# Optimization experiments

Hardware: AMD Instinct MI355X
Metric: run time of the kernel (lower is better)

The kernel has to match this reference:

```python
import jax, jax.numpy as jnp
import numpy as np

S = 2048      # sequence length
D = 2048      # d_model
H = 16        # n_heads
E = 128       # d_head


def setup_inputs() -> dict:
    key = jax.random.key(0)
    kx, kw = jax.random.split(key)
    x = jax.random.normal(kx, (S, D), dtype=jnp.float32)
    # xavier_normal for fan_in=D, fan_out=3*E per head
    std = float(np.sqrt(2.0 / (D + 3 * E)))
    w_qkv = jax.random.normal(kw, (H, D, 3 * E), dtype=jnp.float32) * std
    return {"x": x, "w_qkv": w_qkv}


def reference(x, w_qkv):
    # qkv: [h, s, 3e]
    qkv = jnp.einsum('sd,hde->hse', x, w_qkv)
    q, k, v = jnp.split(qkv, 3, axis=-1)            # each [h, s, e]
    scores = jnp.einsum('hse,hte->hst', q, k) / jnp.sqrt(jnp.asarray(E, x.dtype))
    attn = jax.nn.softmax(scores, axis=-1)          # [h, s, t]
    out = jnp.einsum('hst,hte->hse', attn, v)       # [h, s, e]
    # concat heads: [s, h*e]
    return out.transpose(1, 0, 2).reshape(x.shape[0], -1)
```

## Files before the change

### kernel.cpp

```cpp
#include <hip/hip_runtime.h>

#define SEQ 2048
#define DMODEL 2048
#define NHEAD 16
#define EHEAD 128
#define NE3 384

using short8 = __attribute__((ext_vector_type(8))) short;
using f32x4  = __attribute__((ext_vector_type(4))) float;
using f32x16 = __attribute__((ext_vector_type(16))) float;
using uint4v = __attribute__((ext_vector_type(4))) unsigned int;
using uint2v = __attribute__((ext_vector_type(2))) unsigned int;

__device__ __forceinline__ unsigned short f32_to_bf16(float f) {
    unsigned int u = __float_as_uint(f);
    unsigned int rounding = 0x7fffu + ((u >> 16) & 1u);
    u += rounding;
    return (unsigned short)(u >> 16);
}

__device__ __forceinline__ void async_load16(const void* g, void* l) {
    __builtin_amdgcn_global_load_lds(
        (const __attribute__((address_space(1))) unsigned int*)g,
        (__attribute__((address_space(3))) unsigned int*)l, 16, 0, 0);
}

__global__ void prep_kernel(const float* __restrict__ x, unsigned short* __restrict__ xb,
                            const float* __restrict__ w, unsigned short* __restrict__ wT) {
    __shared__ float tile[64][65];
    const int bid = blockIdx.x;
    if (bid < 4096) {
        int i = (bid * blockDim.x + threadIdx.x) * 4;
        float4 v = *(const float4*)(x + i);
        ushort4 o = make_ushort4(f32_to_bf16(v.x), f32_to_bf16(v.y), f32_to_bf16(v.z), f32_to_bf16(v.w));
        *(ushort4*)(xb + i) = o;
        return;
    }
    const int b = bid - 4096;
    const int h  = b / 192;
    const int r6 = b % 192;
    const int n0 = (r6 / 32) * 64;
    const int d0 = (r6 % 32) * 64;
    int t = threadIdx.x;
    int rr = t >> 4;
    int cc = (t & 15) * 4;
#pragma unroll
    for (int i = 0; i < 4; i++) {
        float4 v = *(const float4*)&w[(size_t)(h * DMODEL + d0 + rr + i * 16) * NE3 + n0 + cc];
        tile[rr + i * 16][cc + 0] = v.x;
        tile[rr + i * 16][cc + 1] = v.y;
        tile[rr + i * 16][cc + 2] = v.z;
        tile[rr + i * 16][cc + 3] = v.w;
    }
    __syncthreads();
#pragma unroll
    for (int i = 0; i < 4; i++) {
        int n = rr + i * 16;
        ushort4 o;
        o.x = f32_to_bf16(tile[cc + 0][n]);
        o.y = f32_to_bf16(tile[cc + 1][n]);
        o.z = f32_to_bf16(tile[cc + 2][n]);
        o.w = f32_to_bf16(tile[cc + 3][n]);
        *(ushort4*)&wT[(size_t)(h * NE3 + n0 + n) * DMODEL + d0 + cc] = o;
    }
}

template <int B, bool STAGE, int VM, bool RDNEXT>
__device__ __forceinline__ void qkv_kstep(
        unsigned short* lds, f32x4 (&acc)[4][6],
        short8 (&aC)[4], short8 (&bC)[3],
        short8 (&aN)[4], short8 (&bN)[3],
        const unsigned short*& p0, const unsigned short*& p1,
        const unsigned short*& p2, const unsigned short*& p3,
        const int d0, const int d1, const int d2, const int d3,
        const int aoff, const int boff) {
    constexpr int CUR = B * 16384;
    constexpr int NXT = ((B + 1) & 3) * 16384;
    constexpr int DST = ((B + 3) & 3) * 16384;

    short8 b1[3];
#pragma unroll
    for (int nf = 0; nf < 3; ++nf) b1[nf] = *(const short8*)(lds + CUR + boff + (3 + nf) * 512);
    if constexpr (STAGE) {
        async_load16(p0, lds + DST + d0);
        async_load16(p1, lds + DST + d1);
    }
    p0 += 32; p1 += 32;
    if constexpr (VM == 6)      asm volatile("s_waitcnt vmcnt(6)");
    else if constexpr (VM == 4) asm volatile("s_waitcnt vmcnt(4)");
    else if constexpr (VM == 0) asm volatile("s_waitcnt vmcnt(0)");
    __builtin_amdgcn_s_barrier();
    __builtin_amdgcn_s_setprio(1);
#pragma unroll
    for (int mf = 0; mf < 4; ++mf)
#pragma unroll
        for (int nf = 0; nf < 3; ++nf)
            acc[mf][nf] = __builtin_amdgcn_mfma_f32_16x16x32_bf16(aC[mf], bC[nf], acc[mf][nf], 0, 0, 0);
    __builtin_amdgcn_s_setprio(0);
    __builtin_amdgcn_s_barrier();

    if constexpr (RDNEXT) {
#pragma unroll
        for (int mf = 0; mf < 4; ++mf) aN[mf] = *(const short8*)(lds + NXT + aoff + mf * 512);
#pragma unroll
        for (int nf = 0; nf < 3; ++nf) bN[nf] = *(const short8*)(lds + NXT + boff + nf * 512);
    }
    if constexpr (STAGE) {
        async_load16(p2, lds + DST + d2);
        async_load16(p3, lds + DST + d3);
    }
    p2 += 32; p3 += 32;
    __builtin_amdgcn_s_barrier();
    __builtin_amdgcn_s_setprio(1);
#pragma unroll
    for (int mf = 0; mf < 4; ++mf)
#pragma unroll
        for (int nf = 0; nf < 3; ++nf)
            acc[mf][3 + nf] = __builtin_amdgcn_mfma_f32_16x16x32_bf16(aC[mf], b1[nf], acc[mf][3 + nf], 0, 0, 0);
    __builtin_amdgcn_s_setprio(0);
    __builtin_amdgcn_s_barrier();
}

__global__ __launch_bounds__(512, 2) void qkv_gemm384(
        const unsigned short* __restrict__ A,
        const unsigned short* __restrict__ Bm,
        unsigned short* __restrict__ Q,
        unsigned short* __restrict__ Kb,
        unsigned short* __restrict__ Vt) {
    extern __shared__ __attribute__((aligned(16))) unsigned short lds[];
    const int mb = blockIdx.x, nb = blockIdx.y;
    const int tid = threadIdx.x;
    const int wave = tid >> 6, lane = tid & 63;
    const int r = lane & 15, q = lane >> 4;
    const int wm = wave >> 2, wn = wave & 3;

    const int rrm  = (tid >> 2) & 15;
    const int kg   = ((tid & 3) ^ ((rrm >> 1) & 3)) * 8;
    const int rowA = ((tid >> 6) << 4) + rrm;
    const unsigned short* p0 = A  + (size_t)(mb * 128 + rowA) * DMODEL + kg;
    const unsigned short* p1 = Bm + (size_t)(nb * 384 + rowA) * DMODEL + kg;
    const unsigned short* p2 = p1 + (size_t)128 * DMODEL;
    const unsigned short* p3 = p1 + (size_t)256 * DMODEL;
    const int d0 = wave * 512;
    const int d1 = 4096 + wave * 512;
    const int d2 = 8192 + wave * 512;
    const int d3 = 12288 + wave * 512;

#pragma unroll
    for (int t = 0; t < 3; ++t) {
        async_load16(p0 + t * 32, lds + t * 16384 + d0);
        async_load16(p1 + t * 32, lds + t * 16384 + d1);
        async_load16(p2 + t * 32, lds + t * 16384 + d2);
        async_load16(p3 + t * 32, lds + t * 16384 + d3);
    }
    p0 += 96; p1 += 96; p2 += 96; p3 += 96;

    const int qs = q ^ ((r >> 1) & 3);
    const int aoff = wm * 2048 + r * 32 + qs * 8;
    const int boff = 4096 + wn * 3072 + r * 32 + qs * 8;

    f32x4 acc[4][6] = {};
    asm volatile("s_waitcnt vmcnt(8)");
    __builtin_amdgcn_s_barrier();

    short8 aA[4], bA[3], aB[4], bB[3];
#pragma unroll
    for (int mf = 0; mf < 4; ++mf) aA[mf] = *(const short8*)(lds + aoff + mf * 512);
#pragma unroll
    for (int nf = 0; nf < 3; ++nf) bA[nf] = *(const short8*)(lds + boff + nf * 512);

    for (int i = 0; i < 15; ++i) {
        qkv_kstep<0, true, 6, true>(lds, acc, aA, bA, aB, bB, p0, p1, p2, p3, d0, d1, d2, d3, aoff, boff);
        qkv_kstep<1, true, 6, true>(lds, acc, aB, bB, aA, bA, p0, p1, p2, p3, d0, d1, d2, d3, aoff, boff);
        qkv_kstep<2, true, 6, true>(lds, acc, aA, bA, aB, bB, p0, p1, p2, p3, d0, d1, d2, d3, aoff, boff);
        qkv_kstep<3, true, 6, true>(lds, acc, aB, bB, aA, bA, p0, p1, p2, p3, d0, d1, d2, d3, aoff, boff);
    }
    qkv_kstep<0, true,  6, true >(lds, acc, aA, bA, aB, bB, p0, p1, p2, p3, d0, d1, d2, d3, aoff, boff);
    qkv_kstep<1, false, 4, true >(lds, acc, aB, bB, aA, bA, p0, p1, p2, p3, d0, d1, d2, d3, aoff, boff);
    qkv_kstep<2, false, 0, true >(lds, acc, aA, bA, aB, bB, p0, p1, p2, p3, d0, d1, d2, d3, aoff, boff);
    qkv_kstep<3, false, -1, false>(lds, acc, aB, bB, aA, bA, p0, p1, p2, p3, d0, d1, d2, d3, aoff, boff);

    const int head = nb;
    const int mbase = mb * 128 + wm * 64;
#pragma unroll
    for (int nf = 0; nf < 6; ++nf) {
        const int cb = wn * 96 + nf * 16;
        const int sel = cb >> 7;
        const int e = (cb & 127) + r;
#pragma unroll
        for (int mf = 0; mf < 4; ++mf) {
            const int row0 = mbase + mf * 16 + q * 4;
            const f32x4 v = acc[mf][nf];
            if (sel == 2) {
                ushort4 o;
                o.x = f32_to_bf16(v[0]);
                o.y = f32_to_bf16(v[1]);
                o.z = f32_to_bf16(v[2]);
                o.w = f32_to_bf16(v[3]);
                *(ushort4*)&Vt[((size_t)head * EHEAD + e) * SEQ + row0] = o;
            } else {
                unsigned short* dst = sel ? Kb : Q;
#pragma unroll
                for (int reg = 0; reg < 4; ++reg)
                    dst[((size_t)head * SEQ + row0 + reg) * EHEAD + e] = f32_to_bf16(v[reg]);
            }
        }
    }
}

__global__ __launch_bounds__(512, 2) void flash_attn(
        const unsigned short* __restrict__ Qg,
        const unsigned short* __restrict__ Kg,
        const unsigned short* __restrict__ Vtg,
        float* __restrict__ out) {
    extern __shared__ __attribute__((aligned(16))) unsigned short lds[];
    unsigned short* sK0 = lds;
    unsigned short* sV0 = lds + 16384;

    const int tid = threadIdx.x;
    const int wave = tid >> 6, lane = tid & 63;
    const int l31 = lane & 31, q2 = lane >> 5;
    const int wm = wave >> 1, wn = wave & 1;
    const int b = blockIdx.x;
    const int h  = (b & 7) + ((b >> 7) << 3);
    const int m0 = ((b >> 3) & 15) * 128;

    const unsigned short* Qh  = Qg  + ((size_t)h * SEQ + m0) * EHEAD;
    const unsigned short* Kh0 = Kg  + (size_t)h * SEQ * EHEAD;
    const unsigned short* Vh  = Vtg + (size_t)h * EHEAD * SEQ;

    const int qkRow = lane >> 4;
    const int qkPos = lane & 15;
    const int vRow  = lane >> 3;
    const int vPos  = lane & 7;

    const unsigned short* gK[2];
    const unsigned short* gV[2];
#pragma unroll
    for (int c = 0; c < 2; c++) {
        int u = wave * 2 + c;
        int row = u * 4 + qkRow;
        int ch = qkPos ^ (row & 7);
        gK[c] = Kh0 + (size_t)row * EHEAD + ch * 8;
        int rv = u * 8 + vRow;
        int cv = vPos ^ (rv & 7);
        gV[c] = Vh + (size_t)rv * SEQ + cv * 8;
        async_load16(gK[c], sK0 + u * 512);
        async_load16(gV[c], sV0 + u * 512);
        gK[c] += 64 * EHEAD;
        gV[c] += 64;
    }

    short8 bq[8];
    {
        const unsigned short* qrow = Qh + (size_t)(wm * 32 + l31) * EHEAD;
#pragma unroll
        for (int kc = 0; kc < 8; kc++)
            bq[kc] = *(const short8*)(qrow + (kc * 2 + q2) * 8);
    }
    __syncthreads();

    const unsigned short* kp[8];
    const unsigned short* vp[8];
    const int rowA = wn * 32 + l31;
#pragma unroll
    for (int kc = 0; kc < 8; kc++)
        kp[kc] = sK0 + rowA * 128 + (((kc * 2 + q2) ^ (rowA & 7)) * 8);
#pragma unroll
    for (int et = 0; et < 4; et++)
#pragma unroll
        for (int kc2 = 0; kc2 < 2; kc2++) {
            int rowV = et * 32 + l31;
            int cch = wn * 4 + kc2 * 2 + q2;
            vp[et * 2 + kc2] = sV0 + rowV * 64 + ((cch ^ (rowV & 7)) * 8);
        }

    const float c1 = 0.12752405856f;
    f32x16 acc_o[4] = {};
    float l_acc0 = 0.f, l_acc1 = 0.f;

    auto body = [&](const int cur, const int nxt, bool pref) {
        if (pref) {
#pragma unroll
            for (int c = 0; c < 2; c++) {
                async_load16(gK[c], sK0 + nxt + (wave * 2 + c) * 512);
                gK[c] += 64 * EHEAD;
            }
#pragma unroll
            for (int c = 0; c < 2; c++) {
                async_load16(gV[c], sV0 + nxt + (wave * 2 + c) * 512);
                gV[c] += 64;
            }
        }

        f32x16 st0 = {}, st1 = {};
        __builtin_amdgcn_s_setprio(1);
#pragma unroll
        for (int kc = 0; kc < 8; kc += 2) {
            short8 ak0 = *(const short8*)(kp[kc] + cur);
            short8 ak1 = *(const short8*)(kp[kc + 1] + cur);
            st0 = __builtin_amdgcn_mfma_f32_32x32x16_bf16(ak0, bq[kc], st0, 0, 0, 0);
            st1 = __builtin_amdgcn_mfma_f32_32x32x16_bf16(ak1, bq[kc + 1], st1, 0, 0, 0);
        }
        __builtin_amdgcn_s_setprio(0);

        unsigned int pk[8];
#pragma unroll
        for (int t = 0; t < 8; t++) {
            float p0 = __builtin_amdgcn_exp2f((st0[2 * t] + st1[2 * t]) * c1);
            float p1 = __builtin_amdgcn_exp2f((st0[2 * t + 1] + st1[2 * t + 1]) * c1);
            l_acc0 += p0;
            l_acc1 += p1;
            unsigned int u0 = __float_as_uint(p0) + 0x8000u;
            unsigned int u1 = __float_as_uint(p1) + 0x8000u;
            pk[t] = __builtin_amdgcn_perm(u1, u0, 0x07060302u);
        }

        short8 fr[2];
#pragma unroll
        for (int kc2 = 0; kc2 < 2; kc2++) {
            unsigned int a0 = pk[kc2 * 4 + 0], a1 = pk[kc2 * 4 + 1];
            unsigned int a2 = pk[kc2 * 4 + 2], a3 = pk[kc2 * 4 + 3];
            uint2v r02 = __builtin_amdgcn_permlane32_swap(a0, a2, false, false);
            uint2v r13 = __builtin_amdgcn_permlane32_swap(a1, a3, false, false);
            uint4v t;
            t.x = r02[0];
            t.y = r13[0];
            t.z = r02[1];
            t.w = r13[1];
            fr[kc2] = __builtin_bit_cast(short8, t);
        }

        __builtin_amdgcn_s_setprio(1);
#pragma unroll
        for (int et = 0; et < 4; et++)
#pragma unroll
            for (int kc2 = 0; kc2 < 2; kc2++) {
                short8 bv = *(const short8*)(vp[et * 2 + kc2] + cur);
                acc_o[et] = __builtin_amdgcn_mfma_f32_32x32x16_bf16(fr[kc2], bv, acc_o[et], 0, 0, 0);
            }
        __builtin_amdgcn_s_setprio(0);
        __syncthreads();
    };

    for (int ip = 0; ip < SEQ / 128; ip++) {
        body(0, 8192, true);
        body(8192, 0, ip != SEQ / 128 - 1);
    }

    float l_acc = l_acc0 + l_acc1;
    l_acc += __shfl_xor(l_acc, 32);

    float* fl = (float*)lds;
#pragma unroll
    for (int et = 0; et < 4; et++) {
        if ((et >> 1) != wn) {
#pragma unroll
            for (int rg = 0; rg < 4; rg++) {
                f32x4 v;
                v[0] = acc_o[et][rg * 4 + 0];
                v[1] = acc_o[et][rg * 4 + 1];
                v[2] = acc_o[et][rg * 4 + 2];
                v[3] = acc_o[et][rg * 4 + 3];
                *(f32x4*)&fl[(size_t)(((wm * 4 + et) * 4 + rg) * 256) + lane * 4] = v;
            }
        }
    }
    fl[16384 + (wm * 2 + wn) * 32 + l31] = l_acc;
    __syncthreads();

    float invq[4][4];
#pragma unroll
    for (int rg = 0; rg < 4; rg++)
#pragma unroll
        for (int i = 0; i < 4; i++) {
            int qy = i + 4 * q2 + 8 * rg;
            float lt = fl[16384 + (wm * 2 + 0) * 32 + qy] + fl[16384 + (wm * 2 + 1) * 32 + qy];
            invq[rg][i] = 1.0f / lt;
        }

#pragma unroll
    for (int et = 0; et < 4; et++) {
        if ((et >> 1) == wn) {
#pragma unroll
            for (int rg = 0; rg < 4; rg++) {
                f32x4 v = *(const f32x4*)&fl[(size_t)(((wm * 4 + et) * 4 + rg) * 256) + lane * 4];
#pragma unroll
                for (int i = 0; i < 4; i++) {
                    int mrow = i + 4 * q2 + 8 * rg;
                    out[(size_t)(m0 + wm * 32 + mrow) * DMODEL + h * EHEAD + et * 32 + l31] =
                        (acc_o[et][rg * 4 + i] + v[i]) * invq[rg][i];
                }
            }
        }
    }
}

extern "C" void kernel_launch(void* const* d_in, const int* in_sizes, int n_in,
                              void* d_out, int out_size, void* d_ws, size_t ws_size,
                              hipStream_t stream) {
    const float* x = (const float*)d_in[0];
    const float* w = (const float*)d_in[1];
    float* out = (float*)d_out;

    char* ws = (char*)d_ws;
    unsigned short* xb = (unsigned short*)(ws);
    unsigned short* wT = (unsigned short*)(ws + 8388608);
    unsigned short* Q  = (unsigned short*)(ws + 33554432);
    unsigned short* Kb = (unsigned short*)(ws + 41943040);
    unsigned short* Vt = (unsigned short*)(ws + 50331648);

    static bool attr_set = false;
    if (!attr_set) {
        hipFuncSetAttribute((const void*)flash_attn,
                            hipFuncAttributeMaxDynamicSharedMemorySize, 66560);
        hipFuncSetAttribute((const void*)qkv_gemm384,
                            hipFuncAttributeMaxDynamicSharedMemorySize, 131072);
        attr_set = true;
    }

    prep_kernel<<<7168, 256, 0, stream>>>(x, xb, w, wT);
    qkv_gemm384<<<dim3(SEQ / 128, NHEAD), 512, 131072, stream>>>(xb, wT, Q, Kb, Vt);
    flash_attn<<<256, 512, 66560, stream>>>(Q, Kb, Vt, out);
}
```

Baseline: 201.9 us.

## Restructure QKV GEMM k-step to one barrier with full-fragment prefetch

The QKV projection k-step drops its two-phase schedule of four barriers per step. It now issues all four async global-to-LDS loads up front, waits once on vmcnt/lgkmcnt, and uses a single barrier. It then prefetches the whole next A and B fragment set, both B halves, into registers before running all 24 MFMAs back to back. This cuts barrier count and lets LDS reads overlap a longer MFMA burst, at the cost of more live registers from the doubled B fragment buffers and a coarser wait granularity.

```diff
diff --git a/kernel.cpp b/kernel.cpp
--- a/kernel.cpp
+++ b/kernel.cpp
@@ -68,57 +68,47 @@
 template <int B, bool STAGE, int VM, bool RDNEXT>
 __device__ __forceinline__ void qkv_kstep(
         unsigned short* lds, f32x4 (&acc)[4][6],
-        short8 (&aC)[4], short8 (&bC)[3],
-        short8 (&aN)[4], short8 (&bN)[3],
+        short8 (&aC)[4], short8 (&b0C)[3], short8 (&b1C)[3],
+        short8 (&aN)[4], short8 (&b0N)[3], short8 (&b1N)[3],
         const unsigned short*& p0, const unsigned short*& p1,
         const unsigned short*& p2, const unsigned short*& p3,
         const int d0, const int d1, const int d2, const int d3,
         const int aoff, const int boff) {
-    constexpr int CUR = B * 16384;
     constexpr int NXT = ((B + 1) & 3) * 16384;
     constexpr int DST = ((B + 3) & 3) * 16384;
 
-    short8 b1[3];
-#pragma unroll
-    for (int nf = 0; nf < 3; ++nf) b1[nf] = *(const short8*)(lds + CUR + boff + (3 + nf) * 512);
     if constexpr (STAGE) {
         async_load16(p0, lds + DST + d0);
         async_load16(p1, lds + DST + d1);
-    }
-    p0 += 32; p1 += 32;
-    if constexpr (VM == 6)      asm volatile("s_waitcnt vmcnt(6)");
+        async_load16(p2, lds + DST + d2);
+        async_load16(p3, lds + DST + d3);
+    }
+    p0 += 32; p1 += 32; p2 += 32; p3 += 32;
+    if constexpr (VM == 8)      asm volatile("s_waitcnt vmcnt(8)");
     else if constexpr (VM == 4) asm volatile("s_waitcnt vmcnt(4)");
     else if constexpr (VM == 0) asm volatile("s_waitcnt vmcnt(0)");
+    asm volatile("s_waitcnt lgkmcnt(0)");
     __builtin_amdgcn_s_barrier();
+    if constexpr (RDNEXT) {
+#pragma unroll
+        for (int mf = 0; mf < 4; ++mf) aN[mf]  = *(const short8*)(lds + NXT + aoff + mf * 512);
+#pragma unroll
+        for (int nf = 0; nf < 3; ++nf) b0N[nf] = *(const short8*)(lds + NXT + boff + nf * 512);
+#pragma unroll
+        for (int nf = 0; nf < 3; ++nf) b1N[nf] = *(const short8*)(lds + NXT + boff + (3 + nf) * 512);
+    }
     __builtin_amdgcn_s_setprio(1);
 #pragma unroll
     for (int mf = 0; mf < 4; ++mf)
 #pragma unroll
         for (int nf = 0; nf < 3; ++nf)
-            acc[mf][nf] = __builtin_amdgcn_mfma_f32_16x16x32_bf16(aC[mf], bC[nf], acc[mf][nf], 0, 0, 0);
+            acc[mf][nf] = __builtin_amdgcn_mfma_f32_16x16x32_bf16(aC[mf], b0C[nf], acc[mf][nf], 0, 0, 0);
+#pragma unroll
+    for (int mf = 0; mf < 4; ++mf)
+#pragma unroll
+        for (int nf = 0; nf < 3; ++nf)
+            acc[mf][3 + nf] = __builtin_amdgcn_mfma_f32_16x16x32_bf16(aC[mf], b1C[nf], acc[mf][3 + nf], 0, 0, 0);
     __builtin_amdgcn_s_setprio(0);
-    __builtin_amdgcn_s_barrier();
-
-    if constexpr (RDNEXT) {
-#pragma unroll
-        for (int mf = 0; mf < 4; ++mf) aN[mf] = *(const short8*)(lds + NXT + aoff + mf * 512);
-#pragma unroll
-        for (int nf = 0; nf < 3; ++nf) bN[nf] = *(const short8*)(lds + NXT + boff + nf * 512);
-    }
-    if constexpr (STAGE) {
-        async_load16(p2, lds + DST + d2);
-        async_load16(p3, lds + DST + d3);
-    }
-    p2 += 32; p3 += 32;
-    __builtin_amdgcn_s_barrier();
-    __builtin_amdgcn_s_setprio(1);
-#pragma unroll
-    for (int mf = 0; mf < 4; ++mf)
-#pragma unroll
-        for (int nf = 0; nf < 3; ++nf)
-            acc[mf][3 + nf] = __builtin_amdgcn_mfma_f32_16x16x32_bf16(aC[mf], b1[nf], acc[mf][3 + nf], 0, 0, 0);
-    __builtin_amdgcn_s_setprio(0);
-    __builtin_amdgcn_s_barrier();
 }
 
 __global__ __launch_bounds__(512, 2) void qkv_gemm384(
@@ -163,22 +153,24 @@
     asm volatile("s_waitcnt vmcnt(8)");
     __builtin_amdgcn_s_barrier();
 
-    short8 aA[4], bA[3], aB[4], bB[3];
-#pragma unroll
-    for (int mf = 0; mf < 4; ++mf) aA[mf] = *(const short8*)(lds + aoff + mf * 512);
-#pragma unroll
-    for (int nf = 0; nf < 3; ++nf) bA[nf] = *(const short8*)(lds + boff + nf * 512);
+    short8 aA[4], b0A[3], b1A[3], aB[4], b0B[3], b1B[3];
+#pragma unroll
+    for (int mf = 0; mf < 4; ++mf) aA[mf]  = *(const short8*)(lds + aoff + mf * 512);
+#pragma unroll
+    for (int nf = 0; nf < 3; ++nf) b0A[nf] = *(const short8*)(lds + boff + nf * 512);
+#pragma unroll
+    for (int nf = 0; nf < 3; ++nf) b1A[nf] = *(const short8*)(lds + boff + (3 + nf) * 512);
 
     for (int i = 0; i < 15; ++i) {
-        qkv_kstep<0, true, 6, true>(lds, acc, aA, bA, aB, bB, p0, p1, p2, p3, d0, d1, d2, d3, aoff, boff);
-        qkv_kstep<1, true, 6, true>(lds, acc, aB, bB, aA, bA, p0, p1, p2, p3, d0, d1, d2, d3, aoff, boff);
-        qkv_kstep<2, true, 6, true>(lds, acc, aA, bA, aB, bB, p0, p1, p2, p3, d0, d1, d2, d3, aoff, boff);
-        qkv_kstep<3, true, 6, true>(lds, acc, aB, bB, aA, bA, p0, p1, p2, p3, d0, d1, d2, d3, aoff, boff);
-    }
-    qkv_kstep<0, true,  6, true >(lds, acc, aA, bA, aB, bB, p0, p1, p2, p3, d0, d1, d2, d3, aoff, boff);
-    qkv_kstep<1, false, 4, true >(lds, acc, aB, bB, aA, bA, p0, p1, p2, p3, d0, d1, d2, d3, aoff, boff);
-    qkv_kstep<2, false, 0, true >(lds, acc, aA, bA, aB, bB, p0, p1, p2, p3, d0, d1, d2, d3, aoff, boff);
-    qkv_kstep<3, false, -1, false>(lds, acc, aB, bB, aA, bA, p0, p1, p2, p3, d0, d1, d2, d3, aoff, boff);
+        qkv_kstep<0, true, 8, true>(lds, acc, aA, b0A, b1A, aB, b0B, b1B, p0, p1, p2, p3, d0, d1, d2, d3, aoff, boff);
+        qkv_kstep<1, true, 8, true>(lds, acc, aB, b0B, b1B, aA, b0A, b1A, p0, p1, p2, p3, d0, d1, d2, d3, aoff, boff);
+        qkv_kstep<2, true, 8, true>(lds, acc, aA, b0A, b1A, aB, b0B, b1B, p0, p1, p2, p3, d0, d1, d2, d3, aoff, boff);
+        qkv_kstep<3, true, 8, true>(lds, acc, aB, b0B, b1B, aA, b0A, b1A, p0, p1, p2, p3, d0, d1, d2, d3, aoff, boff);
+    }
+    qkv_kstep<0, true,  8, true >(lds, acc, aA, b0A, b1A, aB, b0B, b1B, p0, p1, p2, p3, d0, d1, d2, d3, aoff, boff);
+    qkv_kstep<1, false, 4, true >(lds, acc, aB, b0B, b1B, aA, b0A, b1A, p0, p1, p2, p3, d0, d1, d2, d3, aoff, boff);
+    qkv_kstep<2, false, 0, true >(lds, acc, aA, b0A, b1A, aB, b0B, b1B, p0, p1, p2, p3, d0, d1, d2, d3, aoff, boff);
+    qkv_kstep<3, false, -1, false>(lds, acc, aB, b0B, b1B, aA, b0A, b1A, p0, p1, p2, p3, d0, d1, d2, d3, aoff, boff);
 
     const int head = nb;
     const int mbase = mb * 128 + wm * 64;
```

Result: faster. 190.5 us (-5.7%).
